# Kernel optimization log

Hardware: AMD Instinct MI355X
Metric: run time of the kernel (lower is better)

The kernel has to match this reference:

```python
import jax, jax.numpy as jnp
import numpy as np


def setup_inputs() -> dict:
    key = jax.random.key(0)
    kx, ka = jax.random.split(key)
    B, N, D = 8, 4096, 32
    x = jax.random.normal(kx, (B, N, D), dtype=jnp.float32)
    # adjacency-like nonnegative weights (dense branch of GsumLayer)
    a = jax.random.uniform(ka, (B, N, N), dtype=jnp.float32)
    return {"x": x, "a": a}


def reference(x, a):
    # GsumLayer dense branch: out[b] = a[b] @ x[b]  -> [B, N, D]
    return jnp.einsum('bnm,bmd->bnd', a, x)
```

## Files before the change

### kernel.cpp

```cpp
#include <hip/hip_runtime.h>


#define GN 4096
#define GD 32
#define GB 8
#define BK 256
#define NCH (GN / BK)
#define NT 512
#define TILE_N 128
#define PK (BK + 8)

typedef float f32x4 __attribute__((ext_vector_type(4)));
typedef short s16x8 __attribute__((ext_vector_type(8)));

__global__ __launch_bounds__(NT, 2) void gsum_mfma(
    const float* __restrict__ x,
    const float* __restrict__ a,
    float* __restrict__ out)
{
    __shared__ __align__(16) unsigned short Xh[2][GD][PK];
    __shared__ __align__(16) unsigned short Xl[2][GD][PK];

    const int t  = threadIdx.x;
    const int w  = t >> 6;
    const int l  = t & 63;
    const int m  = l & 15;
    const int kg = l >> 4;

    const int b    = blockIdx.x >> 5;
    const int tile = blockIdx.x & 31;
    const int n0   = tile * TILE_N + w * 16;

    const float* Xb = x + (long long)b * GN * GD;
    const float* arow = a + ((long long)b * GN + n0 + m) * GN + kg * 8;

    const int kr = t >> 1;
    const int c0 = (t & 1) * 16;

    f32x4 acc0 = {0.f, 0.f, 0.f, 0.f};
    f32x4 acc1 = {0.f, 0.f, 0.f, 0.f};

    auto XLOAD = [&](int k0, float4* xr) {
        const float* p = Xb + (long long)(k0 + kr) * GD + c0;
        xr[0] = *(const float4*)(p);
        xr[1] = *(const float4*)(p + 4);
        xr[2] = *(const float4*)(p + 8);
        xr[3] = *(const float4*)(p + 12);
    };
    auto XWRITE = [&](int nb, const float4* xr) {
        #pragma unroll
        for (int q = 0; q < 4; ++q) {
            const float fv[4] = {xr[q].x, xr[q].y, xr[q].z, xr[q].w};
            #pragma unroll
            for (int j = 0; j < 4; ++j) {
                const int d = c0 + q * 4 + j;
                unsigned u  = __float_as_uint(fv[j]);
                unsigned hb = (u + 0x8000u) >> 16;
                float hif   = __uint_as_float(hb << 16);
                unsigned lb = (__float_as_uint(fv[j] - hif) + 0x8000u) >> 16;
                Xh[nb][d][kr] = (unsigned short)hb;
                Xl[nb][d][kr] = (unsigned short)lb;
            }
        }
    };
    auto ALOAD = [&](f32x4* dst, int k) {
        const int kc = (k >= GN) ? (k - GN) : k;
        const float* p = arow + kc;
        dst[0] = *(const f32x4*)(p);
        dst[1] = *(const f32x4*)(p + 4);
    };

    {
        float4 xr[4];
        XLOAD(0, xr);
        XWRITE(0, xr);
    }
    f32x4 pa[2][2];
    ALOAD(pa[0], 0);
    ALOAD(pa[1], 32);
    asm volatile("s_waitcnt lgkmcnt(0)" ::: "memory");
    __builtin_amdgcn_s_barrier();

    for (int c = 0; c < NCH; ++c) {
        const int nb = c & 1;
        const int k0 = c * BK;

        float4 xnext[4];
        if (c + 1 < NCH) XLOAD(k0 + BK, xnext);

        #pragma unroll
        for (int s = 0; s < 8; ++s) {
            float av[8];
            #pragma unroll
            for (int e = 0; e < 4; ++e) {
                av[e]     = pa[s & 1][0][e];
                av[4 + e] = pa[s & 1][1][e];
            }
            ALOAD(pa[s & 1], k0 + s * 32 + 64);

            s16x8 ahi, alo;
            #pragma unroll
            for (int e = 0; e < 8; ++e) {
                unsigned u  = __float_as_uint(av[e]);
                unsigned hb = (u + 0x8000u) >> 16;
                ahi[e] = (short)hb;
                float hif = __uint_as_float(hb << 16);
                alo[e] = (short)((__float_as_uint(av[e] - hif) + 0x8000u) >> 16);
            }

            const int kk = s * 32 + kg * 8;
            s16x8 xh0 = *(const s16x8*)&Xh[nb][m][kk];
            s16x8 xl0 = *(const s16x8*)&Xl[nb][m][kk];
            s16x8 xh1 = *(const s16x8*)&Xh[nb][16 + m][kk];
            s16x8 xl1 = *(const s16x8*)&Xl[nb][16 + m][kk];

            acc0 = __builtin_amdgcn_mfma_f32_16x16x32_bf16(xh0, ahi, acc0, 0, 0, 0);
            acc1 = __builtin_amdgcn_mfma_f32_16x16x32_bf16(xh1, ahi, acc1, 0, 0, 0);
            acc0 = __builtin_amdgcn_mfma_f32_16x16x32_bf16(xl0, ahi, acc0, 0, 0, 0);
            acc1 = __builtin_amdgcn_mfma_f32_16x16x32_bf16(xl1, ahi, acc1, 0, 0, 0);
            acc0 = __builtin_amdgcn_mfma_f32_16x16x32_bf16(xh0, alo, acc0, 0, 0, 0);
            acc1 = __builtin_amdgcn_mfma_f32_16x16x32_bf16(xh1, alo, acc1, 0, 0, 0);
        }

        if (c + 1 < NCH) XWRITE((c + 1) & 1, xnext);
        asm volatile("s_waitcnt lgkmcnt(0)" ::: "memory");
        __builtin_amdgcn_s_barrier();
    }

    float* Ob = out + ((long long)b * GN + n0 + m) * GD + kg * 4;
    #pragma unroll
    for (int j = 0; j < 4; ++j) {
        Ob[j]      = acc0[j];
        Ob[16 + j] = acc1[j];
    }
}

extern "C" void kernel_launch(void* const* d_in, const int* in_sizes, int n_in,
                              void* d_out, int out_size, void* d_ws, size_t ws_size,
                              hipStream_t stream) {
    const float* x = (const float*)d_in[0];
    const float* a = (const float*)d_in[1];
    float* out = (float*)d_out;

    dim3 grid(GB * (GN / TILE_N));
    dim3 block(NT);
    gsum_mfma<<<grid, block, 0, stream>>>(x, a, out);
}
```

Baseline: 712.9 us.

## Precompute split-bf16 transposed X in a prep kernel and stage A through LDS

Adds a separate prep kernel that converts x into transposed hi/lo bf16 arrays in workspace, so the main kernel no longer converts X per block or needs a shared X buffer and block barriers. The main kernel now loads A with coalesced row-wise 16-byte loads into a per-wave, XOR-swizzled LDS tile. X fragments come straight from global memory into registers. MFMA operand order is swapped, so the output store layout changes. The cost is an extra launch, more register pressure from st[16] and xf[8][4], and a reliance on explicit sched_barrier ordering instead of cross-wave barriers.

Result: slower. 741.5 us (+4.0%).

```diff
diff --git a/kernel.cpp b/kernel.cpp
--- a/kernel.cpp
+++ b/kernel.cpp
@@ -4,134 +4,161 @@
 #define GN 4096
 #define GD 32
 #define GB 8
-#define BK 256
-#define NCH (GN / BK)
+#define BKC 256
+#define NCH (GN / BKC)
 #define NT 512
+#define NW 8
 #define TILE_N 128
-#define PK (BK + 8)
 
 typedef float f32x4 __attribute__((ext_vector_type(4)));
 typedef short s16x8 __attribute__((ext_vector_type(8)));
 
+__global__ __launch_bounds__(256, 4) void xprep(
+    const float* __restrict__ x,
+    unsigned short* __restrict__ xth,
+    unsigned short* __restrict__ xtl)
+{
+    const int t  = threadIdx.x;
+    const int b  = blockIdx.x >> 5;
+    const int kc = blockIdx.x & 31;
+    const int d  = t & 31;
+    const int kb = t >> 5;
+    const int k0 = kc * 128 + kb * 16;
+    const float* xb = x + (long long)b * GN * GD;
+
+    __attribute__((aligned(16))) unsigned short hi[16];
+    __attribute__((aligned(16))) unsigned short lo[16];
+    #pragma unroll
+    for (int j = 0; j < 16; ++j) {
+        float f = xb[(long long)(k0 + j) * GD + d];
+        unsigned u  = __float_as_uint(f);
+        unsigned hb = (u + 0x8000u) >> 16;
+        float hif   = __uint_as_float(hb << 16);
+        hi[j] = (unsigned short)hb;
+        lo[j] = (unsigned short)((__float_as_uint(f - hif) + 0x8000u) >> 16);
+    }
+    long long ob = ((long long)(b * GD + d)) * GN + k0;
+    *(s16x8*)(xth + ob)     = *(const s16x8*)&hi[0];
+    *(s16x8*)(xth + ob + 8) = *(const s16x8*)&hi[8];
+    *(s16x8*)(xtl + ob)     = *(const s16x8*)&lo[0];
+    *(s16x8*)(xtl + ob + 8) = *(const s16x8*)&lo[8];
+}
+
 __global__ __launch_bounds__(NT, 2) void gsum_mfma(
-    const float* __restrict__ x,
     const float* __restrict__ a,
+    const unsigned short* __restrict__ xth,
+    const unsigned short* __restrict__ xtl,
     float* __restrict__ out)
 {
-    __shared__ __align__(16) unsigned short Xh[2][GD][PK];
-    __shared__ __align__(16) unsigned short Xl[2][GD][PK];
+    __shared__ float As[NW][16][BKC];
 
     const int t  = threadIdx.x;
     const int w  = t >> 6;
     const int l  = t & 63;
     const int m  = l & 15;
     const int kg = l >> 4;
+    const int m7 = m & 7;
 
     const int b    = blockIdx.x >> 5;
     const int tile = blockIdx.x & 31;
     const int n0   = tile * TILE_N + w * 16;
 
-    const float* Xb = x + (long long)b * GN * GD;
-    const float* arow = a + ((long long)b * GN + n0 + m) * GN + kg * 8;
+    const float* Ab = a + ((long long)b * GN + n0) * GN;
+    const unsigned short* xh0p = xth + (long long)(b * GD + m) * GN;
+    const unsigned short* xh1p = xh0p + 16 * GN;
+    const unsigned short* xl0p = xtl + (long long)(b * GD + m) * GN;
+    const unsigned short* xl1p = xl0p + 16 * GN;
+    const int kfo = kg * 8;
 
-    const int kr = t >> 1;
-    const int c0 = (t & 1) * 16;
+    float* lds = &As[w][0][0];
 
     f32x4 acc0 = {0.f, 0.f, 0.f, 0.f};
     f32x4 acc1 = {0.f, 0.f, 0.f, 0.f};
+    s16x8 xf[8][4];
+    f32x4 st[16];
 
-    auto XLOAD = [&](int k0, float4* xr) {
-        const float* p = Xb + (long long)(k0 + kr) * GD + c0;
-        xr[0] = *(const float4*)(p);
-        xr[1] = *(const float4*)(p + 4);
-        xr[2] = *(const float4*)(p + 8);
-        xr[3] = *(const float4*)(p + 12);
+    auto STAGE = [&](int c) {
+        const float* p = Ab + c * BKC + l * 4;
+        #pragma unroll
+        for (int r = 0; r < 16; ++r)
+            st[r] = *(const f32x4*)(p + (long long)r * GN);
     };
-    auto XWRITE = [&](int nb, const float4* xr) {
+    auto DSWRITE = [&]() {
         #pragma unroll
-        for (int q = 0; q < 4; ++q) {
-            const float fv[4] = {xr[q].x, xr[q].y, xr[q].z, xr[q].w};
+        for (int r = 0; r < 16; ++r)
+            *(f32x4*)(lds + r * BKC + ((l ^ (r & 7)) * 4)) = st[r];
+    };
+    auto FRAGS = [&](int c) {
+        #pragma unroll
+        for (int s = 0; s < 8; ++s) {
+            const long long k = (long long)c * BKC + s * 32 + kfo;
+            xf[s][0] = *(const s16x8*)(xh0p + k);
+            xf[s][1] = *(const s16x8*)(xh1p + k);
+            xf[s][2] = *(const s16x8*)(xl0p + k);
+            xf[s][3] = *(const s16x8*)(xl1p + k);
+        }
+    };
+    auto COMPUTE = [&]() {
+        #pragma unroll
+        for (int s = 0; s < 8; ++s) {
+            const int g0 = (((s * 8 + kg * 2)     ^ m7) * 4);
+            const int g1 = (((s * 8 + kg * 2 + 1) ^ m7) * 4);
+            f32x4 fa = *(const f32x4*)(lds + m * BKC + g0);
+            f32x4 fb = *(const f32x4*)(lds + m * BKC + g1);
+            s16x8 ahi, alo;
             #pragma unroll
-            for (int j = 0; j < 4; ++j) {
-                const int d = c0 + q * 4 + j;
-                unsigned u  = __float_as_uint(fv[j]);
-                unsigned hb = (u + 0x8000u) >> 16;
-                float hif   = __uint_as_float(hb << 16);
-                unsigned lb = (__float_as_uint(fv[j] - hif) + 0x8000u) >> 16;
-                Xh[nb][d][kr] = (unsigned short)hb;
-                Xl[nb][d][kr] = (unsigned short)lb;
+            for (int e = 0; e < 4; ++e) {
+                {
+                    unsigned u  = __float_as_uint(fa[e]);
+                    unsigned hb = (u + 0x8000u) >> 16;
+                    ahi[e] = (short)hb;
+                    float hif = __uint_as_float(hb << 16);
+                    alo[e] = (short)((__float_as_uint(fa[e] - hif) + 0x8000u) >> 16);
+                }
+                {
+                    unsigned u  = __float_as_uint(fb[e]);
+                    unsigned hb = (u + 0x8000u) >> 16;
+                    ahi[4 + e] = (short)hb;
+                    float hif = __uint_as_float(hb << 16);
+                    alo[4 + e] = (short)((__float_as_uint(fb[e] - hif) + 0x8000u) >> 16);
+                }
+            }
+            acc0 = __builtin_amdgcn_mfma_f32_16x16x32_bf16(ahi, xf[s][0], acc0, 0, 0, 0);
+            acc1 = __builtin_amdgcn_mfma_f32_16x16x32_bf16(ahi, xf[s][1], acc1, 0, 0, 0);
+            acc0 = __builtin_amdgcn_mfma_f32_16x16x32_bf16(alo, xf[s][0], acc0, 0, 0, 0);
+            acc1 = __builtin_amdgcn_mfma_f32_16x16x32_bf16(alo, xf[s][1], acc1, 0, 0, 0);
+            acc0 = __builtin_amdgcn_mfma_f32_16x16x32_bf16(ahi, xf[s][2], acc0, 0, 0, 0);
+            acc1 = __builtin_amdgcn_mfma_f32_16x16x32_bf16(ahi, xf[s][3], acc1, 0, 0, 0);
+        }
+    };
+
+    STAGE(0);
+    DSWRITE();
+    FRAGS(0);
+    __builtin_amdgcn_sched_barrier(0);
+    STAGE(1);
+    __builtin_amdgcn_sched_barrier(0);
+
+    for (int c = 0; c < NCH; ++c) {
+        COMPUTE();
+        __builtin_amdgcn_sched_barrier(0);
+        if (c + 1 < NCH) {
+            DSWRITE();
+            __builtin_amdgcn_sched_barrier(0);
+            FRAGS(c + 1);
+            __builtin_amdgcn_sched_barrier(0);
+            if (c + 2 < NCH) {
+                STAGE(c + 2);
+                __builtin_amdgcn_sched_barrier(0);
             }
         }
-    };
-    auto ALOAD = [&](f32x4* dst, int k) {
-        const int kc = (k >= GN) ? (k - GN) : k;
-        const float* p = arow + kc;
-        dst[0] = *(const f32x4*)(p);
-        dst[1] = *(const f32x4*)(p + 4);
-    };
-
-    {
-        float4 xr[4];
-        XLOAD(0, xr);
-        XWRITE(0, xr);
-    }
-    f32x4 pa[2][2];
-    ALOAD(pa[0], 0);
-    ALOAD(pa[1], 32);
-    asm volatile("s_waitcnt lgkmcnt(0)" ::: "memory");
-    __builtin_amdgcn_s_barrier();
-
-    for (int c = 0; c < NCH; ++c) {
-        const int nb = c & 1;
-        const int k0 = c * BK;
-
-        float4 xnext[4];
-        if (c + 1 < NCH) XLOAD(k0 + BK, xnext);
-
-        #pragma unroll
-        for (int s = 0; s < 8; ++s) {
-            float av[8];
-            #pragma unroll
-            for (int e = 0; e < 4; ++e) {
-                av[e]     = pa[s & 1][0][e];
-                av[4 + e] = pa[s & 1][1][e];
-            }
-            ALOAD(pa[s & 1], k0 + s * 32 + 64);
-
-            s16x8 ahi, alo;
-            #pragma unroll
-            for (int e = 0; e < 8; ++e) {
-                unsigned u  = __float_as_uint(av[e]);
-                unsigned hb = (u + 0x8000u) >> 16;
-                ahi[e] = (short)hb;
-                float hif = __uint_as_float(hb << 16);
-                alo[e] = (short)((__float_as_uint(av[e] - hif) + 0x8000u) >> 16);
-            }
-
-            const int kk = s * 32 + kg * 8;
-            s16x8 xh0 = *(const s16x8*)&Xh[nb][m][kk];
-            s16x8 xl0 = *(const s16x8*)&Xl[nb][m][kk];
-            s16x8 xh1 = *(const s16x8*)&Xh[nb][16 + m][kk];
-            s16x8 xl1 = *(const s16x8*)&Xl[nb][16 + m][kk];
-
-            acc0 = __builtin_amdgcn_mfma_f32_16x16x32_bf16(xh0, ahi, acc0, 0, 0, 0);
-            acc1 = __builtin_amdgcn_mfma_f32_16x16x32_bf16(xh1, ahi, acc1, 0, 0, 0);
-            acc0 = __builtin_amdgcn_mfma_f32_16x16x32_bf16(xl0, ahi, acc0, 0, 0, 0);
-            acc1 = __builtin_amdgcn_mfma_f32_16x16x32_bf16(xl1, ahi, acc1, 0, 0, 0);
-            acc0 = __builtin_amdgcn_mfma_f32_16x16x32_bf16(xh0, alo, acc0, 0, 0, 0);
-            acc1 = __builtin_amdgcn_mfma_f32_16x16x32_bf16(xh1, alo, acc1, 0, 0, 0);
-        }
-
-        if (c + 1 < NCH) XWRITE((c + 1) & 1, xnext);
-        asm volatile("s_waitcnt lgkmcnt(0)" ::: "memory");
-        __builtin_amdgcn_s_barrier();
     }
 
-    float* Ob = out + ((long long)b * GN + n0 + m) * GD + kg * 4;
+    float* Ob = out + ((long long)b * GN + n0) * GD;
     #pragma unroll
     for (int j = 0; j < 4; ++j) {
-        Ob[j]      = acc0[j];
-        Ob[16 + j] = acc1[j];
+        Ob[(kg * 4 + j) * GD + m]      = acc0[j];
+        Ob[(kg * 4 + j) * GD + 16 + m] = acc1[j];
     }
 }
 
@@ -142,7 +169,9 @@
     const float* a = (const float*)d_in[1];
     float* out = (float*)d_out;
 
-    dim3 grid(GB * (GN / TILE_N));
-    dim3 block(NT);
-    gsum_mfma<<<grid, block, 0, stream>>>(x, a, out);
+    unsigned short* xth = (unsigned short*)d_ws;
+    unsigned short* xtl = xth + (long long)GB * GD * GN;
+
+    xprep<<<dim3(GB * 32), dim3(256), 0, stream>>>(x, xth, xtl);
+    gsum_mfma<<<dim3(GB * (GN / TILE_N)), dim3(NT), 0, stream>>>(a, xth, xtl, out);
 }
```
